# Kernel optimization log

Hardware: AMD Instinct MI355X
Metric: run time of the kernel (lower is better)

## Reference

```python
import jax, jax.numpy as jnp
import numpy as np

ALPHA = 0.2  # LeakyReLU negative slope
NEG_INF = -1e9


def setup_inputs() -> dict:
    key = jax.random.key(0)
    k1, k2, k3, k4 = jax.random.split(key, 4)
    B, N, Fin, Fout = 8, 2048, 128, 64
    h = jax.random.normal(k1, (B, N, Fin), dtype=jnp.float32)
    adj_mask = jax.random.randint(k2, (B, N, N), 0, 2).astype(jnp.int32)
    # xavier_uniform-style scales
    W = jax.random.uniform(k3, (Fout, Fin), dtype=jnp.float32,
                           minval=-1.0, maxval=1.0) * np.sqrt(6.0 / (Fin + Fout))
    a = jax.random.uniform(k4, (2 * Fout,), dtype=jnp.float32,
                           minval=-1.0, maxval=1.0) * np.sqrt(6.0 / (2 * Fout + 1))
    return {"h": h, "adj_mask": adj_mask, "W": W, "a": a}


def reference(h, adj_mask, W, a):
    # Wh: [B, N, Fout]
    Wh = jnp.einsum("bnf,of->bno", h, W)
    Fout = Wh.shape[-1]
    a1, a2 = a[:Fout], a[Fout:]
    # additive decomposition of a([Wh_i || Wh_j]): e_ij = leakyrelu(s1_i + s2_j)
    s1 = Wh @ a1  # [B, N]
    s2 = Wh @ a2  # [B, N]
    e = jax.nn.leaky_relu(s1[:, :, None] + s2[:, None, :], negative_slope=ALPHA)  # [B,N,N]
    e = jnp.where(adj_mask == 0, NEG_INF, e)
    attention = jax.nn.softmax(e, axis=-1)
    # dropout is identity in eval mode / p effectively 0 for the reference
    h_prime = jnp.einsum("bij,bjo->bio", attention, Wh)
    return h_prime
```

## Files before the change

### kernel.cpp

```cpp
#include <hip/hip_runtime.h>
#include <math.h>

#define LRELU_ALPHA 0.2f
#define NEG_INF -1000000000.0f

constexpr int B_ = 8, N_ = 2048, FIN = 128, FOUT = 64;

typedef __attribute__((ext_vector_type(8))) short bf16x8;
typedef __attribute__((ext_vector_type(4))) float f32x4;

__global__ __launch_bounds__(256) void k_wh(
    const float* __restrict__ h, const float* __restrict__ W,
    const float* __restrict__ a,
    unsigned short* __restrict__ WhT_hi, unsigned short* __restrict__ WhT_lo,
    float* __restrict__ s1, float* __restrict__ s2) {
  __shared__ float Wt[128][65];
  __shared__ float hs[16][128];

  const int t = threadIdx.x;
  const int row0 = blockIdx.x * 16;

  for (int e = t; e < 64 * 128; e += 256) {
    int o = e >> 7, f = e & 127;
    Wt[f][o] = W[e];
  }
  {
    const float4* hg = (const float4*)(h + (size_t)row0 * FIN);
    for (int i4 = t; i4 < 16 * 32; i4 += 256) {
      int r = i4 >> 5, f4 = i4 & 31;
      *(float4*)&hs[r][f4 * 4] = hg[i4];
    }
  }
  __syncthreads();

  const int wave = t >> 6, lane = t & 63;
  float acc[4] = {0.f, 0.f, 0.f, 0.f};
#pragma unroll 4
  for (int f4 = 0; f4 < 32; ++f4) {
    float w0 = Wt[4 * f4 + 0][lane], w1 = Wt[4 * f4 + 1][lane];
    float w2 = Wt[4 * f4 + 2][lane], w3 = Wt[4 * f4 + 3][lane];
#pragma unroll
    for (int r = 0; r < 4; ++r) {
      float4 hv = *(const float4*)&hs[wave * 4 + r][f4 * 4];
      acc[r] += hv.x * w0 + hv.y * w1 + hv.z * w2 + hv.w * w3;
    }
  }

  const float a1v = a[lane], a2v = a[64 + lane];
  const int b = row0 / N_;
#pragma unroll
  for (int r = 0; r < 4; ++r) {
    const int row = row0 + wave * 4 + r;
    const int n = row - b * N_;
    const float v = acc[r];
    unsigned int u = __float_as_uint(v) & 0xFFFF0000u;
    float lo = v - __uint_as_float(u);
    size_t base = ((size_t)b * 64 + lane) * N_ + n;
    WhT_hi[base] = (unsigned short)(u >> 16);
    WhT_lo[base] = (unsigned short)(__float_as_uint(lo) >> 16);
    float p1 = v * a1v, p2 = v * a2v;
#pragma unroll
    for (int d = 32; d; d >>= 1) {
      p1 += __shfl_xor(p1, d, 64);
      p2 += __shfl_xor(p2, d, 64);
    }
    if (lane == 0) { s1[row] = p1; s2[row] = p2; }
  }
}

__global__ __launch_bounds__(256, 4) void k_attn(
    const unsigned short* __restrict__ WhT_hi,
    const unsigned short* __restrict__ WhT_lo,
    const float* __restrict__ s1g, const float* __restrict__ s2g,
    const int* __restrict__ adj, float* __restrict__ out) {
  __shared__ float acc_lds[4][64][16];
  __shared__ float lsum_lds[4][16];

  const int t = threadIdx.x;
  const int wave = t >> 6, lane = t & 63;
  const int b = blockIdx.y;
  const int i0 = blockIdx.x * 16;
  const int m = lane & 15, q = lane >> 4;

  const float s1r = s1g[b * N_ + i0 + m];
  const int jbase = wave * (N_ / 4);
  const int* adjR = adj + ((size_t)b * N_ + i0 + m) * (size_t)N_;
  const float* s2R = s2g + b * N_;
  const unsigned short* whh = WhT_hi + (size_t)b * 64 * N_;
  const unsigned short* whl = WhT_lo + (size_t)b * 64 * N_;

  f32x4 acc0 = {0.f, 0.f, 0.f, 0.f}, acc1 = acc0, acc2 = acc0, acc3 = acc0;
  float lsum = 0.f;

  for (int c = 0; c < 16; ++c) {
    const int jq = jbase + c * 32 + q * 8;
    int4 av0 = *(const int4*)(adjR + jq);
    int4 av1 = *(const int4*)(adjR + jq + 4);
    float4 sv0 = *(const float4*)(s2R + jq);
    float4 sv1 = *(const float4*)(s2R + jq + 4);

    float xs[8] = {sv0.x, sv0.y, sv0.z, sv0.w, sv1.x, sv1.y, sv1.z, sv1.w};
    int avs[8] = {av0.x, av0.y, av0.z, av0.w, av1.x, av1.y, av1.z, av1.w};

    bf16x8 ah, al;
#pragma unroll
    for (int j = 0; j < 8; ++j) {
      float x = s1r + xs[j];
      float e = fmaxf(x, LRELU_ALPHA * x);
      e = avs[j] ? e : NEG_INF;
      float p = __expf(e);
      lsum += p;
      unsigned int u = __float_as_uint(p) & 0xFFFF0000u;
      ah[j] = (short)(u >> 16);
      float lo = p - __uint_as_float(u);
      al[j] = (short)(__float_as_uint(lo) >> 16);
    }

#pragma unroll
    for (int g = 0; g < 4; ++g) {
      const size_t boff = (size_t)(g * 16 + m) * N_ + jq;
      bf16x8 bh = *(const bf16x8*)(whh + boff);
      bf16x8 bl = *(const bf16x8*)(whl + boff);
      f32x4& acc = (g == 0) ? acc0 : (g == 1) ? acc1 : (g == 2) ? acc2 : acc3;
      acc = __builtin_amdgcn_mfma_f32_16x16x32_bf16(ah, bh, acc, 0, 0, 0);
      acc = __builtin_amdgcn_mfma_f32_16x16x32_bf16(ah, bl, acc, 0, 0, 0);
      acc = __builtin_amdgcn_mfma_f32_16x16x32_bf16(al, bh, acc, 0, 0, 0);
    }
  }

  lsum += __shfl_xor(lsum, 16, 64);
  lsum += __shfl_xor(lsum, 32, 64);
  if (lane < 16) lsum_lds[wave][lane] = lsum;

  *(f32x4*)&acc_lds[wave][lane][0]  = acc0;
  *(f32x4*)&acc_lds[wave][lane][4]  = acc1;
  *(f32x4*)&acc_lds[wave][lane][8]  = acc2;
  *(f32x4*)&acc_lds[wave][lane][12] = acc3;
  __syncthreads();

#pragma unroll
  for (int kk = 0; kk < 4; ++kk) {
    int e = kk * 256 + t;
    int row = e >> 6, o = e & 63;
    int src_lane = (o & 15) | ((row >> 2) << 4);
    int slot = (o >> 4) * 4 + (row & 3);
    float v = acc_lds[0][src_lane][slot] + acc_lds[1][src_lane][slot] +
              acc_lds[2][src_lane][slot] + acc_lds[3][src_lane][slot];
    float l = lsum_lds[0][row] + lsum_lds[1][row] +
              lsum_lds[2][row] + lsum_lds[3][row];
    if (l == 0.f) l = 1.f;
    out[((size_t)b * N_ + i0 + row) * FOUT + o] = v / l;
  }
}

extern "C" void kernel_launch(void* const* d_in, const int* in_sizes, int n_in,
                              void* d_out, int out_size, void* d_ws, size_t ws_size,
                              hipStream_t stream) {
  const float* h   = (const float*)d_in[0];
  const int*   adj = (const int*)d_in[1];
  const float* W   = (const float*)d_in[2];
  const float* a   = (const float*)d_in[3];
  float* out = (float*)d_out;

  unsigned short* WhT_hi = (unsigned short*)d_ws;
  unsigned short* WhT_lo = WhT_hi + (size_t)B_ * 64 * N_;
  float* s1 = (float*)(WhT_lo + (size_t)B_ * 64 * N_);
  float* s2 = s1 + (size_t)B_ * N_;

  k_wh<<<dim3(B_ * N_ / 16), 256, 0, stream>>>(h, W, a, WhT_hi, WhT_lo, s1, s2);
  k_attn<<<dim3(N_ / 16, B_), 256, 0, stream>>>(WhT_hi, WhT_lo, s1, s2, adj, out);
}
```

Before: 269.7 us.

## Switch attention to single fp16 MFMA with LDS double-buffered async staging

Replaces the three-pass bf16 hi/lo split with a single fp16 representation of Wh and probabilities, cutting MFMA work and Wh traffic. The attention kernel now handles 32 rows per block, with waves specialised: two waves load adjacency tiles and two load Wh tiles via global_load_lds into double-buffered shared memory. s2 is cached in LDS, and the exponent is shifted by a constant to limit fp16 overflow. This gives up precision, since fp16 probabilities and Wh lose mantissa bits relative to the split-bf16 scheme, and it lowers occupancy.

New measurement: 226.2 us. -16.1%, faster.

```diff
diff --git a/kernel.cpp b/kernel.cpp
--- a/kernel.cpp
+++ b/kernel.cpp
@@ -1,4 +1,5 @@
 #include <hip/hip_runtime.h>
+#include <hip/hip_fp16.h>
 #include <math.h>
 
 #define LRELU_ALPHA 0.2f
@@ -6,13 +7,18 @@
 
 constexpr int B_ = 8, N_ = 2048, FIN = 128, FOUT = 64;
 
-typedef __attribute__((ext_vector_type(8))) short bf16x8;
-typedef __attribute__((ext_vector_type(4))) float f32x4;
+typedef _Float16 __attribute__((ext_vector_type(8))) f16x8;
+typedef float __attribute__((ext_vector_type(4))) f32x4;
+
+__device__ __forceinline__ void gload16(const void* g, void* l) {
+  __builtin_amdgcn_global_load_lds(
+      (const __attribute__((address_space(1))) void*)g,
+      (__attribute__((address_space(3))) void*)l, 16, 0, 0);
+}
 
 __global__ __launch_bounds__(256) void k_wh(
     const float* __restrict__ h, const float* __restrict__ W,
-    const float* __restrict__ a,
-    unsigned short* __restrict__ WhT_hi, unsigned short* __restrict__ WhT_lo,
+    const float* __restrict__ a, unsigned short* __restrict__ WhT,
     float* __restrict__ s1, float* __restrict__ s2) {
   __shared__ float Wt[128][65];
   __shared__ float hs[16][128];
@@ -53,11 +59,7 @@
     const int row = row0 + wave * 4 + r;
     const int n = row - b * N_;
     const float v = acc[r];
-    unsigned int u = __float_as_uint(v) & 0xFFFF0000u;
-    float lo = v - __uint_as_float(u);
-    size_t base = ((size_t)b * 64 + lane) * N_ + n;
-    WhT_hi[base] = (unsigned short)(u >> 16);
-    WhT_lo[base] = (unsigned short)(__float_as_uint(lo) >> 16);
+    WhT[((size_t)b * 64 + lane) * N_ + n] = __half_as_ushort(__float2half(v));
     float p1 = v * a1v, p2 = v * a2v;
 #pragma unroll
     for (int d = 32; d; d >>= 1) {
@@ -68,89 +70,116 @@
   }
 }
 
-__global__ __launch_bounds__(256, 4) void k_attn(
-    const unsigned short* __restrict__ WhT_hi,
-    const unsigned short* __restrict__ WhT_lo,
+__global__ __launch_bounds__(256, 2) void k_attn(
+    const unsigned short* __restrict__ WhT,
     const float* __restrict__ s1g, const float* __restrict__ s2g,
     const int* __restrict__ adj, float* __restrict__ out) {
-  __shared__ float acc_lds[4][64][16];
-  __shared__ float lsum_lds[4][16];
+  __shared__ __align__(16) unsigned char sA[16 * 1024];
+  __shared__ __align__(16) unsigned char sB[16 * 1024];
+  __shared__ float s2s[N_];
+  __shared__ float lsum_lds[32];
 
   const int t = threadIdx.x;
   const int wave = t >> 6, lane = t & 63;
+  const int m = lane & 15, q = lane >> 4;
   const int b = blockIdx.y;
-  const int i0 = blockIdx.x * 16;
-  const int m = lane & 15, q = lane >> 4;
-
-  const float s1r = s1g[b * N_ + i0 + m];
-  const int jbase = wave * (N_ / 4);
-  const int* adjR = adj + ((size_t)b * N_ + i0 + m) * (size_t)N_;
+  const int i0 = blockIdx.x * 32;
+  const int rg = wave & 1;
+  const int p0 = (wave >> 1) * 2;
+
+  const int* adjB = adj + (size_t)b * N_ * N_;
+  const unsigned short* whB = WhT + (size_t)b * 64 * N_;
   const float* s2R = s2g + b * N_;
-  const unsigned short* whh = WhT_hi + (size_t)b * 64 * N_;
-  const unsigned short* whl = WhT_lo + (size_t)b * 64 * N_;
-
-  f32x4 acc0 = {0.f, 0.f, 0.f, 0.f}, acc1 = acc0, acc2 = acc0, acc3 = acc0;
+
+  for (int i = t; i < N_ / 4; i += 256)
+    ((float4*)s2s)[i] = ((const float4*)s2R)[i];
+
+  const float s1r = s1g[b * N_ + i0 + rg * 16 + m];
+
+  const unsigned char* gp[4];
+  int gstr;
+  if (wave < 2) {
+    const size_t r = (size_t)(i0 + wave * 16 + m);
+#pragma unroll
+    for (int ii = 0; ii < 4; ++ii) {
+      int ks = ii >> 1, hh = ii & 1;
+      gp[ii] = (const unsigned char*)(adjB + r * N_ + ks * 32 + q * 8 + hh * 4);
+    }
+    gstr = 64 * 4;
+  } else {
+#pragma unroll
+    for (int ii = 0; ii < 4; ++ii) {
+      int g = (wave - 2) * 2 + (ii >> 1), ks = ii & 1;
+      gp[ii] = (const unsigned char*)(whB + (size_t)(g * 16 + m) * N_ +
+                                      ks * 32 + q * 8);
+    }
+    gstr = 64 * 2;
+  }
+
+#define STAGE(S, c)                                                       \
+  {                                                                       \
+    _Pragma("unroll") for (int ii = 0; ii < 4; ++ii)                      \
+        gload16(gp[ii] + (size_t)(c) * gstr, (S) + (wave * 4 + ii) * 1024); \
+  }
+
+  f32x4 acc0 = {0.f, 0.f, 0.f, 0.f}, acc1 = acc0;
   float lsum = 0.f;
 
-  for (int c = 0; c < 16; ++c) {
-    const int jq = jbase + c * 32 + q * 8;
-    int4 av0 = *(const int4*)(adjR + jq);
-    int4 av1 = *(const int4*)(adjR + jq + 4);
-    float4 sv0 = *(const float4*)(s2R + jq);
-    float4 sv1 = *(const float4*)(s2R + jq + 4);
-
-    float xs[8] = {sv0.x, sv0.y, sv0.z, sv0.w, sv1.x, sv1.y, sv1.z, sv1.w};
-    int avs[8] = {av0.x, av0.y, av0.z, av0.w, av1.x, av1.y, av1.z, av1.w};
-
-    bf16x8 ah, al;
-#pragma unroll
-    for (int j = 0; j < 8; ++j) {
-      float x = s1r + xs[j];
-      float e = fmaxf(x, LRELU_ALPHA * x);
-      e = avs[j] ? e : NEG_INF;
-      float p = __expf(e);
-      lsum += p;
-      unsigned int u = __float_as_uint(p) & 0xFFFF0000u;
-      ah[j] = (short)(u >> 16);
-      float lo = p - __uint_as_float(u);
-      al[j] = (short)(__float_as_uint(lo) >> 16);
-    }
-
-#pragma unroll
-    for (int g = 0; g < 4; ++g) {
-      const size_t boff = (size_t)(g * 16 + m) * N_ + jq;
-      bf16x8 bh = *(const bf16x8*)(whh + boff);
-      bf16x8 bl = *(const bf16x8*)(whl + boff);
-      f32x4& acc = (g == 0) ? acc0 : (g == 1) ? acc1 : (g == 2) ? acc2 : acc3;
-      acc = __builtin_amdgcn_mfma_f32_16x16x32_bf16(ah, bh, acc, 0, 0, 0);
-      acc = __builtin_amdgcn_mfma_f32_16x16x32_bf16(ah, bl, acc, 0, 0, 0);
-      acc = __builtin_amdgcn_mfma_f32_16x16x32_bf16(al, bh, acc, 0, 0, 0);
-    }
+  auto consume = [&](const unsigned char* base, int c) {
+#pragma unroll
+    for (int ks = 0; ks < 2; ++ks) {
+      int4 A0 = *(const int4*)(base + (rg * 4 + ks * 2 + 0) * 1024 + lane * 16);
+      int4 A1 = *(const int4*)(base + (rg * 4 + ks * 2 + 1) * 1024 + lane * 16);
+      const float* sp = &s2s[c * 64 + ks * 32 + q * 8];
+      float4 sv0 = *(const float4*)sp;
+      float4 sv1 = *(const float4*)(sp + 4);
+      float xs[8] = {sv0.x, sv0.y, sv0.z, sv0.w, sv1.x, sv1.y, sv1.z, sv1.w};
+      int avs[8] = {A0.x, A0.y, A0.z, A0.w, A1.x, A1.y, A1.z, A1.w};
+      f16x8 af;
+#pragma unroll
+      for (int j = 0; j < 8; ++j) {
+        float x = s1r + xs[j];
+        float e = fmaxf(x, LRELU_ALPHA * x);
+        e = avs[j] ? (e - 2.0f) : NEG_INF;
+        float p = __expf(e);
+        lsum += p;
+        af[j] = (_Float16)p;
+      }
+      f16x8 b0 = *(const f16x8*)(base + (8 + (p0 + 0) * 2 + ks) * 1024 + lane * 16);
+      f16x8 b1 = *(const f16x8*)(base + (8 + (p0 + 1) * 2 + ks) * 1024 + lane * 16);
+      acc0 = __builtin_amdgcn_mfma_f32_16x16x32_f16(af, b0, acc0, 0, 0, 0);
+      acc1 = __builtin_amdgcn_mfma_f32_16x16x32_f16(af, b1, acc1, 0, 0, 0);
+    }
+  };
+
+  STAGE(sA, 0);
+  __syncthreads();
+
+  for (int cc = 0; cc < 16; ++cc) {
+    const int c0 = 2 * cc, c1 = 2 * cc + 1;
+    STAGE(sB, c1);
+    consume(sA, c0);
+    __syncthreads();
+    if (c1 + 1 < 32) STAGE(sA, c1 + 1);
+    consume(sB, c1);
+    __syncthreads();
   }
 
   lsum += __shfl_xor(lsum, 16, 64);
   lsum += __shfl_xor(lsum, 32, 64);
-  if (lane < 16) lsum_lds[wave][lane] = lsum;
-
-  *(f32x4*)&acc_lds[wave][lane][0]  = acc0;
-  *(f32x4*)&acc_lds[wave][lane][4]  = acc1;
-  *(f32x4*)&acc_lds[wave][lane][8]  = acc2;
-  *(f32x4*)&acc_lds[wave][lane][12] = acc3;
+  if (wave < 2 && lane < 16) lsum_lds[wave * 16 + lane] = lsum;
   __syncthreads();
 
 #pragma unroll
-  for (int kk = 0; kk < 4; ++kk) {
-    int e = kk * 256 + t;
-    int row = e >> 6, o = e & 63;
-    int src_lane = (o & 15) | ((row >> 2) << 4);
-    int slot = (o >> 4) * 4 + (row & 3);
-    float v = acc_lds[0][src_lane][slot] + acc_lds[1][src_lane][slot] +
-              acc_lds[2][src_lane][slot] + acc_lds[3][src_lane][slot];
-    float l = lsum_lds[0][row] + lsum_lds[1][row] +
-              lsum_lds[2][row] + lsum_lds[3][row];
-    if (l == 0.f) l = 1.f;
-    out[((size_t)b * N_ + i0 + row) * FOUT + o] = v / l;
-  }
+  for (int r = 0; r < 4; ++r) {
+    const int ri = q * 4 + r;
+    float l = lsum_lds[rg * 16 + ri];
+    float inv = (l == 0.f) ? 1.f : 1.f / l;
+    const size_t row = (size_t)b * N_ + i0 + rg * 16 + ri;
+    out[row * FOUT + (p0 + 0) * 16 + m] = acc0[r] * inv;
+    out[row * FOUT + (p0 + 1) * 16 + m] = acc1[r] * inv;
+  }
+#undef STAGE
 }
 
 extern "C" void kernel_launch(void* const* d_in, const int* in_sizes, int n_in,
@@ -162,11 +191,10 @@
   const float* a   = (const float*)d_in[3];
   float* out = (float*)d_out;
 
-  unsigned short* WhT_hi = (unsigned short*)d_ws;
-  unsigned short* WhT_lo = WhT_hi + (size_t)B_ * 64 * N_;
-  float* s1 = (float*)(WhT_lo + (size_t)B_ * 64 * N_);
+  unsigned short* WhT = (unsigned short*)d_ws;
+  float* s1 = (float*)(WhT + (size_t)B_ * 64 * N_);
   float* s2 = s1 + (size_t)B_ * N_;
 
-  k_wh<<<dim3(B_ * N_ / 16), 256, 0, stream>>>(h, W, a, WhT_hi, WhT_lo, s1, s2);
-  k_attn<<<dim3(N_ / 16, B_), 256, 0, stream>>>(WhT_hi, WhT_lo, s1, s2, adj, out);
-}
+  k_wh<<<dim3(B_ * N_ / 16), 256, 0, stream>>>(h, W, a, WhT, s1, s2);
+  k_attn<<<dim3(N_ / 32, B_), 256, 0, stream>>>(WhT, s1, s2, adj, out);
+}
```
